# Optimization experiments

Measured on AMD Instinct MI355X. Metric: run time of the kernel, lower is better.

## Reference

```python
import jax, jax.numpy as jnp
import numpy as np

NUM_RELS = 8


def rgcn_conv(x, src, tgt, etype, W, root, bias, num_rels):
    """PyG-style RGCNConv: out_i = x_i @ root + bias
                              + sum_r mean_{j in N_r(i)} x_j @ W_r
    Aggregate-then-transform (valid since W_r is linear) to avoid
    materializing per-edge transformed messages.
    x: [N, Din], src/tgt/etype: [E], W: [R, Din, Dout], root: [Din, Dout].
    """
    N = x.shape[0]
    # combined segment id over (target node, relation)
    seg = tgt.astype(jnp.int32) * num_rels + etype.astype(jnp.int32)  # [E]
    msgs = x[src]  # [E, Din] gather
    agg = jax.ops.segment_sum(msgs, seg, num_segments=N * num_rels)  # [N*R, Din]
    cnt = jax.ops.segment_sum(jnp.ones((src.shape[0],), x.dtype), seg,
                              num_segments=N * num_rels)  # [N*R]
    agg = agg / jnp.maximum(cnt, 1.0)[:, None]  # mean aggregation per relation
    agg = agg.reshape(N, num_rels, -1)  # [N, R, Din]
    out = jnp.einsum('nri,rio->no', agg, W)
    out = out + x @ root + bias
    return out


def setup_inputs() -> dict:
    key = jax.random.key(0)
    ks = jax.random.split(key, 9)
    N, E, R = 100000, 1600000, NUM_RELS
    Din, Dh, Dout = 128, 128, 64
    x = jax.random.normal(ks[0], (N, Din), dtype=jnp.float32)
    edge_index = jax.random.randint(ks[1], (2, E), 0, N, dtype=jnp.int32)
    edge_type = jax.random.randint(ks[2], (E,), 0, R, dtype=jnp.int32)
    s1 = 1.0 / np.sqrt(Din)
    s2 = 1.0 / np.sqrt(Dh)
    W1 = jax.random.uniform(ks[3], (R, Din, Dh), jnp.float32, -s1, s1)
    root1 = jax.random.uniform(ks[4], (Din, Dh), jnp.float32, -s1, s1)
    b1 = jnp.zeros((Dh,), jnp.float32)
    W2 = jax.random.uniform(ks[5], (R, Dh, Dout), jnp.float32, -s2, s2)
    root2 = jax.random.uniform(ks[6], (Dh, Dout), jnp.float32, -s2, s2)
    b2 = jnp.zeros((Dout,), jnp.float32)
    return {"x": x, "edge_index": edge_index, "edge_type": edge_type,
            "W1": W1, "root1": root1, "b1": b1,
            "W2": W2, "root2": root2, "b2": b2}


def reference(x, edge_index, edge_type, W1, root1, b1, W2, root2, b2):
    src, tgt = edge_index[0], edge_index[1]
    h = rgcn_conv(x, src, tgt, edge_type, W1, root1, b1, NUM_RELS)
    h = jax.nn.relu(h)
    # dropout is identity in eval mode
    out = rgcn_conv(h, src, tgt, edge_type, W2, root2, b2, NUM_RELS)
    return out
```

## Files before the change

kernel.cpp:

```cpp
#include <hip/hip_runtime.h>
#include <cstdint>
#include <cstddef>


#define DIN 128
#define NREL 8
#define SCAN_BLK 256
#define SCAN_ITEMS 16
#define SCAN_CHUNK (SCAN_BLK * SCAN_ITEMS)

typedef short bf16x8 __attribute__((ext_vector_type(8)));
typedef float f32x4 __attribute__((ext_vector_type(4)));

__device__ inline float bf2f(short s) {
  return __uint_as_float(((unsigned int)(unsigned short)s) << 16);
}
__device__ inline short f2bf(float f) {
  unsigned int u = __float_as_uint(f);
  unsigned int r = (u + 0x7FFFu + ((u >> 16) & 1u)) >> 16;
  return (short)r;
}

__global__ void zero_ints(int4* __restrict__ p, int n4) {
  int i = blockIdx.x * blockDim.x + threadIdx.x;
  int stride = gridDim.x * blockDim.x;
  int4 z; z.x = z.y = z.z = z.w = 0;
  for (; i < n4; i += stride) p[i] = z;
}

__global__ void hist_kernel(const int* __restrict__ tgt, const int* __restrict__ et,
                            int* __restrict__ hist, int E, int N) {
  int i = blockIdx.x * blockDim.x + threadIdx.x;
  int stride = gridDim.x * blockDim.x;
  for (; i < E; i += stride)
    atomicAdd(&hist[et[i] * N + tgt[i]], 1);
}

__global__ void scanA(const int* __restrict__ hist, int* __restrict__ partials, int RN) {
  __shared__ int sh[SCAN_BLK];
  const int tid = threadIdx.x;
  int base = blockIdx.x * SCAN_CHUNK + tid * SCAN_ITEMS;
  int s = 0;
  #pragma unroll
  for (int j = 0; j < SCAN_ITEMS; ++j) {
    int i = base + j;
    s += (i < RN) ? hist[i] : 0;
  }
  sh[tid] = s;
  __syncthreads();
  for (int off = SCAN_BLK / 2; off > 0; off >>= 1) {
    if (tid < off) sh[tid] += sh[tid + off];
    __syncthreads();
  }
  if (tid == 0) partials[blockIdx.x] = sh[0];
}

__global__ void scanB(int* __restrict__ partials, int nblk) {
  int acc = 0;
  for (int i = 0; i < nblk; ++i) {
    int v = partials[i];
    partials[i] = acc;
    acc += v;
  }
}

__global__ void scanC(const int* __restrict__ hist, const int* __restrict__ partials,
                      int* __restrict__ starts, int RN) {
  __shared__ int sh[SCAN_BLK];
  const int tid = threadIdx.x;
  int base = blockIdx.x * SCAN_CHUNK + tid * SCAN_ITEMS;
  int loc[SCAN_ITEMS];
  int s = 0;
  #pragma unroll
  for (int j = 0; j < SCAN_ITEMS; ++j) {
    int i = base + j;
    int v = (i < RN) ? hist[i] : 0;
    loc[j] = s;
    s += v;
  }
  sh[tid] = s;
  __syncthreads();
  for (int off = 1; off < SCAN_BLK; off <<= 1) {
    int v = (tid >= off) ? sh[tid - off] : 0;
    __syncthreads();
    sh[tid] += v;
    __syncthreads();
  }
  int texcl = (tid ? sh[tid - 1] : 0) + partials[blockIdx.x];
  #pragma unroll
  for (int j = 0; j < SCAN_ITEMS; ++j) {
    int i = base + j;
    if (i < RN) starts[i] = texcl + loc[j];
  }
}

__global__ void scatter_fill(const int* __restrict__ src, const int* __restrict__ tgt,
                             const int* __restrict__ et, int* __restrict__ starts,
                             int* __restrict__ sortedsrc, int E, int N) {
  int i = blockIdx.x * blockDim.x + threadIdx.x;
  int stride = gridDim.x * blockDim.x;
  for (; i < E; i += stride) {
    int key = et[i] * N + tgt[i];
    int pos = atomicAdd(&starts[key], 1);
    sortedsrc[pos] = src[i];
  }
}

__global__ void f32_to_bf16(const float* __restrict__ in, short* __restrict__ out, int n8) {
  int i = blockIdx.x * blockDim.x + threadIdx.x;
  int stride = gridDim.x * blockDim.x;
  for (; i < n8; i += stride) {
    const float* p = in + (size_t)i * 8;
    float4 a = *(const float4*)p;
    float4 b = *(const float4*)(p + 4);
    bf16x8 o;
    o[0] = f2bf(a.x); o[1] = f2bf(a.y); o[2] = f2bf(a.z); o[3] = f2bf(a.w);
    o[4] = f2bf(b.x); o[5] = f2bf(b.y); o[6] = f2bf(b.z); o[7] = f2bf(b.w);
    *(bf16x8*)(out + (size_t)i * 8) = o;
  }
}

__global__ void w_conv(const float* __restrict__ W, const float* __restrict__ root,
                       short* __restrict__ WtT, int dout) {
  int total = 9 * dout * 128;
  int i = blockIdx.x * blockDim.x + threadIdx.x;
  int stride = gridDim.x * blockDim.x;
  for (; i < total; i += stride) {
    int p = i / (dout * 128);
    int rem = i - p * dout * 128;
    int o = rem >> 7;
    int k = rem & 127;
    float v = (p < 8) ? W[((size_t)p * 128 + k) * dout + o]
                      : root[(size_t)k * dout + o];
    WtT[i] = f2bf(v);
  }
}

template <int DOUT, bool OUT_BF16_RELU>
__launch_bounds__(256, 4)
__global__ void rgcn_layer(const short* __restrict__ Xb, const short* __restrict__ WtT,
                           const int* __restrict__ sortedsrc, const int* __restrict__ starts,
                           const int* __restrict__ hist, const float* __restrict__ bias,
                           void* __restrict__ outv, int N) {
  constexpr int WC = DOUT / 16;
  const int tid = threadIdx.x;
  const int wid = tid >> 6;
  const int lane = tid & 63;
  const int lr = lane & 15;
  const int kg = (lane >> 4) * 8;
  const int row = blockIdx.x * 64 + wid * 16 + lr;
  const bool rowok = row < N;

  f32x4 acc[WC];
  #pragma unroll
  for (int ni = 0; ni < WC; ++ni) acc[ni] = (f32x4){0.f, 0.f, 0.f, 0.f};

  #pragma unroll 1
  for (int p = 0; p < 9; ++p) {
    bf16x8 af[4];
    if (p == 8) {
      #pragma unroll
      for (int kk = 0; kk < 4; ++kk) {
        bf16x8 v = {0, 0, 0, 0, 0, 0, 0, 0};
        if (rowok) v = *(const bf16x8*)(Xb + (size_t)row * DIN + kk * 32 + kg);
        af[kk] = v;
      }
    } else {
      float ga[4][8];
      #pragma unroll
      for (int kk = 0; kk < 4; ++kk)
        #pragma unroll
        for (int j = 0; j < 8; ++j) ga[kk][j] = 0.f;
      if (rowok) {
        const int key = p * N + row;
        const int end = starts[key];
        const int cnt = hist[key];
        for (int e = end - cnt; e < end; ++e) {
          int s = sortedsrc[e];
          const short* xp = Xb + (size_t)s * DIN + kg;
          #pragma unroll
          for (int kk = 0; kk < 4; ++kk) {
            bf16x8 v = *(const bf16x8*)(xp + kk * 32);
            #pragma unroll
            for (int j = 0; j < 8; ++j) ga[kk][j] += bf2f(v[j]);
          }
        }
        const float sc = 1.0f / fmaxf((float)cnt, 1.0f);
        #pragma unroll
        for (int kk = 0; kk < 4; ++kk)
          #pragma unroll
          for (int j = 0; j < 8; ++j) ga[kk][j] *= sc;
      }
      #pragma unroll
      for (int kk = 0; kk < 4; ++kk) {
        bf16x8 o;
        #pragma unroll
        for (int j = 0; j < 8; ++j) o[j] = f2bf(ga[kk][j]);
        af[kk] = o;
      }
    }
    const short* Wp = WtT + (size_t)p * DOUT * 128;
    #pragma unroll
    for (int kk = 0; kk < 4; ++kk) {
      #pragma unroll
      for (int ni = 0; ni < WC; ++ni) {
        bf16x8 b = *(const bf16x8*)(Wp + (size_t)(ni * 16 + lr) * 128 + kk * 32 + kg);
        acc[ni] = __builtin_amdgcn_mfma_f32_16x16x32_bf16(af[kk], b, acc[ni], 0, 0, 0);
      }
    }
  }

  const int rbase = (lane >> 4) * 4;
  const int orow0 = blockIdx.x * 64 + wid * 16 + rbase;
  #pragma unroll
  for (int ni = 0; ni < WC; ++ni) {
    const int col = ni * 16 + lr;
    const float bcol = bias[col];
    #pragma unroll
    for (int r = 0; r < 4; ++r) {
      const int rr = orow0 + r;
      if (rr >= N) continue;
      float v = acc[ni][r] + bcol;
      if (OUT_BF16_RELU) {
        v = fmaxf(v, 0.f);
        ((short*)outv)[(size_t)rr * DOUT + col] = f2bf(v);
      } else {
        ((float*)outv)[(size_t)rr * DOUT + col] = v;
      }
    }
  }
}

extern "C" void kernel_launch(void* const* d_in, const int* in_sizes, int n_in,
                              void* d_out, int out_size, void* d_ws, size_t ws_size,
                              hipStream_t stream) {
  const float* x     = (const float*)d_in[0];
  const int*   ei    = (const int*)d_in[1];
  const int*   et    = (const int*)d_in[2];
  const float* W1    = (const float*)d_in[3];
  const float* root1 = (const float*)d_in[4];
  const float* b1    = (const float*)d_in[5];
  const float* W2    = (const float*)d_in[6];
  const float* root2 = (const float*)d_in[7];
  const float* b2    = (const float*)d_in[8];
  float* out = (float*)d_out;

  const int N = in_sizes[0] / DIN;
  const int E = in_sizes[1] / 2;
  const int* src = ei;
  const int* tgt = ei + E;
  const int RN = N * NREL;

  char* ws = (char*)d_ws;
  size_t off = 0;
  auto take = [&](size_t bytes) { char* p = ws + off; off += (bytes + 255) & ~(size_t)255; return p; };
  int*   hist      = (int*)take((size_t)RN * 4);
  int*   starts    = (int*)take((size_t)RN * 4);
  int*   partials  = (int*)take(1024);
  int*   sortedsrc = (int*)take((size_t)E * 4);
  short* xb        = (short*)take((size_t)N * DIN * 2);
  short* hb        = (short*)take((size_t)N * DIN * 2);
  short* WtT1      = (short*)take((size_t)9 * 128 * 128 * 2);
  short* WtT2      = (short*)take((size_t)9 * 64 * 128 * 2);

  const int gbl = (N + 63) / 64;
  const int nblkA = (RN + SCAN_CHUNK - 1) / SCAN_CHUNK;

  zero_ints<<<(RN / 4 + 255) / 256, 256, 0, stream>>>((int4*)hist, RN / 4);
  hist_kernel<<<2048, 256, 0, stream>>>(tgt, et, hist, E, N);
  scanA<<<nblkA, SCAN_BLK, 0, stream>>>(hist, partials, RN);
  scanB<<<1, 1, 0, stream>>>(partials, nblkA);
  scanC<<<nblkA, SCAN_BLK, 0, stream>>>(hist, partials, starts, RN);
  scatter_fill<<<2048, 256, 0, stream>>>(src, tgt, et, starts, sortedsrc, E, N);

  w_conv<<<576, 256, 0, stream>>>(W1, root1, WtT1, 128);
  w_conv<<<288, 256, 0, stream>>>(W2, root2, WtT2, 64);
  f32_to_bf16<<<2048, 256, 0, stream>>>(x, xb, N * DIN / 8);

  rgcn_layer<128, true><<<gbl, 256, 0, stream>>>(
      xb, WtT1, sortedsrc, starts, hist, b1, hb, N);
  rgcn_layer<64, false><<<gbl, 256, 0, stream>>>(
      hb, WtT2, sortedsrc, starts, hist, b2, out, N);
}
```

Before: 885.2 us.

## Split relation panels across waves and reduce partial outputs through shared memory

Each block now handles 16 rows instead of 64. Its four waves each process two of the eight relation panels for the same rows, wave 0 also does the root panel, and the four partial accumulators are summed through LDS before a vectorized bias, ReLU and store epilogue. The aim is more parallelism in the latency-bound gather loop, since each wave walks fewer edge lists and four times as many blocks are in flight. In exchange the block uses LDS and a __syncthreads, the work is uneven because wave 0 does an extra panel, and weight panel loads are repeated across four times as many blocks.

```diff
diff --git a/kernel.cpp b/kernel.cpp
--- a/kernel.cpp
+++ b/kernel.cpp
@@ -136,6 +136,52 @@
   }
 }
 
+template <int DOUT>
+__device__ __forceinline__ void panel_mfma(
+    int p, const short* __restrict__ Xb, const short* __restrict__ WtT,
+    const int* __restrict__ sortedsrc, const int* __restrict__ starts,
+    const int* __restrict__ hist, int row, bool rowok, int lr, int kg, int N,
+    f32x4* acc) {
+  constexpr int WC = DOUT / 16;
+  float ga[4][8];
+  #pragma unroll
+  for (int kk = 0; kk < 4; ++kk)
+    #pragma unroll
+    for (int j = 0; j < 8; ++j) ga[kk][j] = 0.f;
+  if (rowok) {
+    const int key = p * N + row;
+    const int end = starts[key];
+    const int cnt = hist[key];
+    for (int e = end - cnt; e < end; ++e) {
+      int s = sortedsrc[e];
+      const short* xp = Xb + (size_t)s * DIN + kg;
+      #pragma unroll
+      for (int kk = 0; kk < 4; ++kk) {
+        bf16x8 v = *(const bf16x8*)(xp + kk * 32);
+        #pragma unroll
+        for (int j = 0; j < 8; ++j) ga[kk][j] += bf2f(v[j]);
+      }
+    }
+    const float sc = 1.0f / fmaxf((float)cnt, 1.0f);
+    #pragma unroll
+    for (int kk = 0; kk < 4; ++kk)
+      #pragma unroll
+      for (int j = 0; j < 8; ++j) ga[kk][j] *= sc;
+  }
+  const short* Wp = WtT + (size_t)p * DOUT * 128;
+  #pragma unroll
+  for (int kk = 0; kk < 4; ++kk) {
+    bf16x8 af;
+    #pragma unroll
+    for (int j = 0; j < 8; ++j) af[j] = f2bf(ga[kk][j]);
+    #pragma unroll
+    for (int ni = 0; ni < WC; ++ni) {
+      bf16x8 b = *(const bf16x8*)(Wp + (size_t)(ni * 16 + lr) * 128 + kk * 32 + kg);
+      acc[ni] = __builtin_amdgcn_mfma_f32_16x16x32_bf16(af, b, acc[ni], 0, 0, 0);
+    }
+  }
+}
+
 template <int DOUT, bool OUT_BF16_RELU>
 __launch_bounds__(256, 4)
 __global__ void rgcn_layer(const short* __restrict__ Xb, const short* __restrict__ WtT,
@@ -143,90 +189,68 @@
                            const int* __restrict__ hist, const float* __restrict__ bias,
                            void* __restrict__ outv, int N) {
   constexpr int WC = DOUT / 16;
+  constexpr int STR = DOUT + 4;
+  __shared__ __align__(16) float Cs[4][16][STR];
   const int tid = threadIdx.x;
   const int wid = tid >> 6;
   const int lane = tid & 63;
   const int lr = lane & 15;
   const int kg = (lane >> 4) * 8;
-  const int row = blockIdx.x * 64 + wid * 16 + lr;
+  const int row0 = blockIdx.x * 16;
+  const int row = row0 + lr;
   const bool rowok = row < N;
 
   f32x4 acc[WC];
   #pragma unroll
   for (int ni = 0; ni < WC; ++ni) acc[ni] = (f32x4){0.f, 0.f, 0.f, 0.f};
 
-  #pragma unroll 1
-  for (int p = 0; p < 9; ++p) {
-    bf16x8 af[4];
-    if (p == 8) {
-      #pragma unroll
-      for (int kk = 0; kk < 4; ++kk) {
-        bf16x8 v = {0, 0, 0, 0, 0, 0, 0, 0};
-        if (rowok) v = *(const bf16x8*)(Xb + (size_t)row * DIN + kk * 32 + kg);
-        af[kk] = v;
-      }
-    } else {
-      float ga[4][8];
-      #pragma unroll
-      for (int kk = 0; kk < 4; ++kk)
-        #pragma unroll
-        for (int j = 0; j < 8; ++j) ga[kk][j] = 0.f;
-      if (rowok) {
-        const int key = p * N + row;
-        const int end = starts[key];
-        const int cnt = hist[key];
-        for (int e = end - cnt; e < end; ++e) {
-          int s = sortedsrc[e];
-          const short* xp = Xb + (size_t)s * DIN + kg;
-          #pragma unroll
-          for (int kk = 0; kk < 4; ++kk) {
-            bf16x8 v = *(const bf16x8*)(xp + kk * 32);
-            #pragma unroll
-            for (int j = 0; j < 8; ++j) ga[kk][j] += bf2f(v[j]);
-          }
-        }
-        const float sc = 1.0f / fmaxf((float)cnt, 1.0f);
-        #pragma unroll
-        for (int kk = 0; kk < 4; ++kk)
-          #pragma unroll
-          for (int j = 0; j < 8; ++j) ga[kk][j] *= sc;
-      }
-      #pragma unroll
-      for (int kk = 0; kk < 4; ++kk) {
-        bf16x8 o;
-        #pragma unroll
-        for (int j = 0; j < 8; ++j) o[j] = f2bf(ga[kk][j]);
-        af[kk] = o;
-      }
-    }
-    const short* Wp = WtT + (size_t)p * DOUT * 128;
+  panel_mfma<DOUT>(wid, Xb, WtT, sortedsrc, starts, hist, row, rowok, lr, kg, N, acc);
+  panel_mfma<DOUT>(wid + 4, Xb, WtT, sortedsrc, starts, hist, row, rowok, lr, kg, N, acc);
+
+  if (wid == 0) {
+    const short* Wp = WtT + (size_t)8 * DOUT * 128;
     #pragma unroll
     for (int kk = 0; kk < 4; ++kk) {
+      bf16x8 af = {0, 0, 0, 0, 0, 0, 0, 0};
+      if (rowok) af = *(const bf16x8*)(Xb + (size_t)row * DIN + kk * 32 + kg);
       #pragma unroll
       for (int ni = 0; ni < WC; ++ni) {
         bf16x8 b = *(const bf16x8*)(Wp + (size_t)(ni * 16 + lr) * 128 + kk * 32 + kg);
-        acc[ni] = __builtin_amdgcn_mfma_f32_16x16x32_bf16(af[kk], b, acc[ni], 0, 0, 0);
+        acc[ni] = __builtin_amdgcn_mfma_f32_16x16x32_bf16(af, b, acc[ni], 0, 0, 0);
       }
     }
   }
 
   const int rbase = (lane >> 4) * 4;
-  const int orow0 = blockIdx.x * 64 + wid * 16 + rbase;
-  #pragma unroll
-  for (int ni = 0; ni < WC; ++ni) {
-    const int col = ni * 16 + lr;
-    const float bcol = bias[col];
-    #pragma unroll
-    for (int r = 0; r < 4; ++r) {
-      const int rr = orow0 + r;
-      if (rr >= N) continue;
-      float v = acc[ni][r] + bcol;
-      if (OUT_BF16_RELU) {
-        v = fmaxf(v, 0.f);
-        ((short*)outv)[(size_t)rr * DOUT + col] = f2bf(v);
-      } else {
-        ((float*)outv)[(size_t)rr * DOUT + col] = v;
-      }
+  #pragma unroll
+  for (int ni = 0; ni < WC; ++ni)
+    #pragma unroll
+    for (int r = 0; r < 4; ++r)
+      Cs[wid][rbase + r][ni * 16 + lr] = acc[ni][r];
+  __syncthreads();
+
+  constexpr int TOT = 16 * DOUT;
+  #pragma unroll
+  for (int base = tid * 4; base < TOT; base += 256 * 4) {
+    const int rrow = base / DOUT;
+    const int col = base % DOUT;
+    float4 s = *(const float4*)&Cs[0][rrow][col];
+    #pragma unroll
+    for (int w = 1; w < 4; ++w) {
+      float4 t = *(const float4*)&Cs[w][rrow][col];
+      s.x += t.x; s.y += t.y; s.z += t.z; s.w += t.w;
+    }
+    float4 bv = *(const float4*)(bias + col);
+    s.x += bv.x; s.y += bv.y; s.z += bv.z; s.w += bv.w;
+    const int rr = row0 + rrow;
+    if (rr >= N) continue;
+    if (OUT_BF16_RELU) {
+      short4 o;
+      o.x = f2bf(fmaxf(s.x, 0.f)); o.y = f2bf(fmaxf(s.y, 0.f));
+      o.z = f2bf(fmaxf(s.z, 0.f)); o.w = f2bf(fmaxf(s.w, 0.f));
+      *(short4*)((short*)outv + (size_t)rr * DOUT + col) = o;
+    } else {
+      *(float4*)((float*)outv + (size_t)rr * DOUT + col) = s;
     }
   }
 }
@@ -263,7 +287,7 @@
   short* WtT1      = (short*)take((size_t)9 * 128 * 128 * 2);
   short* WtT2      = (short*)take((size_t)9 * 64 * 128 * 2);
 
-  const int gbl = (N + 63) / 64;
+  const int gbl = (N + 15) / 16;
   const int nblkA = (RN + SCAN_CHUNK - 1) / SCAN_CHUNK;
 
   zero_ints<<<(RN / 4 + 255) / 256, 256, 0, stream>>>((int4*)hist, RN / 4);
```

Measured after the change: 793.1 us. 10.4% less time.
